# Performance work log

Hardware: AMD Instinct MI355X
Metric: run time of the kernel (lower is better)

## Reference

```python
import jax, jax.numpy as jnp
import numpy as np

N_NODES = 100000


def gcn_layer(x, ei, W, b):
    # PyG GCNConv with add_self_loops=True, edge_weight=None (all ones)
    N = x.shape[0]
    loops = jnp.arange(N, dtype=ei.dtype)
    src = jnp.concatenate([ei[0], loops])
    dst = jnp.concatenate([ei[1], loops])
    h = x @ W  # [N, out_dim]
    ones = jnp.ones(src.shape[0], dtype=x.dtype)
    deg = jax.ops.segment_sum(ones, dst, num_segments=N)
    dinv = jnp.where(deg > 0, jax.lax.rsqrt(deg), 0.0)
    norm = dinv[src] * dinv[dst]  # [E+N]
    msgs = norm[:, None] * h[src]
    out = jax.ops.segment_sum(msgs, dst, num_segments=N)
    return out + b


def forward_once(x, ei, W1, b1, W2, b2):
    h = jax.nn.relu(gcn_layer(x, ei, W1, b1))
    # Dropout(0.25) is identity in eval mode
    z = gcn_layer(h, ei, W2, b2)
    return z  # [N, embed_dim]


def setup_inputs() -> dict:
    key = jax.random.key(0)
    k = jax.random.split(key, 6)
    feat_dim, hidden_dim, embed_dim = 128, 32, 16
    R, E = 4, 1600000
    x = jax.random.normal(k[0], (N_NODES, feat_dim), dtype=jnp.float32)
    eis = jax.random.randint(k[1], (R, 2, E), 0, N_NODES, dtype=jnp.int32)
    s1 = 1.0 / np.sqrt(feat_dim)
    s2 = 1.0 / np.sqrt(hidden_dim)
    W1 = jax.random.uniform(k[2], (feat_dim, hidden_dim), jnp.float32, -s1, s1)
    b1 = jax.random.uniform(k[3], (hidden_dim,), jnp.float32, -s1, s1)
    W2 = jax.random.uniform(k[4], (hidden_dim, embed_dim), jnp.float32, -s2, s2)
    b2 = jax.random.uniform(k[5], (embed_dim,), jnp.float32, -s2, s2)
    return {"x": x, "eis": eis, "W1": W1, "b1": b1, "W2": W2, "b2": b2}


def reference(x, eis, W1, b1, W2, b2):
    # vectorize the per-relation loop over the leading R axis of eis
    embeds = jax.vmap(lambda ei: forward_once(x, ei, W1, b1, W2, b2))(eis)
    # default reduce: embeds.sum(dim=2) on [R, N, embed_dim] -> [R, N]
    return embeds.sum(axis=2)
```

## Files before the change

kernel.cpp:

```cpp
#include <hip/hip_runtime.h>


constexpr int N    = 100000;
constexpr int E    = 1600000;
constexpr int R    = 4;
constexpr int FEAT = 128;
constexpr int HID  = 32;
constexpr int EMB  = 16;
constexpr int M    = R * N;
constexpr int BS   = 256;
constexpr int SH    = 9;
constexpr int BSPAN = 1 << SH;
constexpr int NBUCK = (N + BSPAN - 1) / BSPAN;
constexpr int CH    = 4096;
constexpr int EPT   = CH / BS;
constexpr int NBKr  = (E + CH - 1) / CH;
constexpr int RB    = R * NBUCK;
constexpr int CAP   = 8960;
constexpr int SPT   = (CAP + BSPAN - 1) / BSPAN;
constexpr int OCAP  = 1536;
constexpr int FIX   = 16;
constexpr int GNB   = 64;
constexpr int XPITCH = 132;

typedef _Float16 half8 __attribute__((ext_vector_type(8)));
typedef _Float16 half2v __attribute__((ext_vector_type(2)));

__global__ __launch_bounds__(BS)
void k_gemm_h0(const float* __restrict__ x, const float* __restrict__ W1,
               _Float16* __restrict__ H0h) {
    __shared__ float xs[GNB * XPITCH];
    int base = blockIdx.x * GNB;
    int tid  = threadIdx.x;
#pragma unroll
    for (int u = 0; u < 8; ++u) {
        int f = tid + u * BS;
        int n = f >> 5;
        int c = f & 31;
        if (base + n < N) {
            float4 v = ((const float4*)(x + (size_t)(base + n) * FEAT))[c];
            int p = c ^ ((n & 7) << 2);
            *(float4*)&xs[n * XPITCH + p * 4] = v;
        }
    }
    __syncthreads();
    int oct = __builtin_amdgcn_readfirstlane(tid >> 6);
    int l   = tid & 63;
    int i   = base + l;
    const float* wp = W1 + oct * 8;
    float acc[8];
#pragma unroll
    for (int kk = 0; kk < 8; ++kk) acc[kk] = 0.f;
#pragma unroll 4
    for (int c = 0; c < 32; ++c) {
        int p = c ^ ((l & 7) << 2);
        float4 xv = *(const float4*)&xs[l * XPITCH + p * 4];
        float xk[4] = {xv.x, xv.y, xv.z, xv.w};
#pragma unroll
        for (int dk = 0; dk < 4; ++dk) {
            const float* wr = wp + (c * 4 + dk) * HID;
#pragma unroll
            for (int j = 0; j < 8; ++j)
                acc[j] = fmaf(xk[dk], wr[j], acc[j]);
        }
    }
    half8 hv;
#pragma unroll
    for (int kk = 0; kk < 8; ++kk) hv[kk] = (_Float16)acc[kk];
    if (i < N) ((half8*)H0h)[i * 4 + oct] = hv;
}

__global__ void k_wrow(const float* __restrict__ W2, const float* __restrict__ b2,
                       float* __restrict__ wrowbuf, _Float16* __restrict__ Hsc) {
    int j = threadIdx.x;
    if (j < HID) {
        float s = 0.f;
#pragma unroll
        for (int k = 0; k < EMB; ++k) s += W2[j * EMB + k];
        wrowbuf[j] = s;
    } else if (j == HID) {
        float s = 0.f;
#pragma unroll
        for (int k = 0; k < EMB; ++k) s += b2[k];
        wrowbuf[HID] = s;
    } else if (j >= 34 && j < 50) {
        ((unsigned*)(Hsc + (size_t)M * HID))[j - 34] = 0u;
    }
}

__global__ void k_scat2(const int* __restrict__ eis, int* __restrict__ gcur,
                        int* __restrict__ binned) {
    __shared__ int hist[NBUCK], lstart[NBUCK], cursor[NBUCK], gbase[NBUCK];
    __shared__ int wpart[BS / 64];
    __shared__ int shuf[CH];
    __shared__ unsigned char bkt[CH];
    int r = blockIdx.x / NBKr, k = blockIdx.x - r * NBKr;
    const int* srcp = eis + (size_t)r * 2 * E;
    const int* dstp = srcp + E;
    int e0 = k * CH, n = min(CH, E - e0);
    int tid = threadIdx.x;

    int dreg[EPT], sreg[EPT];
    if (n == CH) {
#pragma unroll
        for (int u = 0; u < EPT; ++u) {
            dreg[u] = dstp[e0 + tid + u * BS];
            sreg[u] = srcp[e0 + tid + u * BS];
        }
    } else {
#pragma unroll
        for (int u = 0; u < EPT; ++u) {
            int i = tid + u * BS;
            dreg[u] = (i < n) ? dstp[e0 + i] : -1;
            sreg[u] = (i < n) ? srcp[e0 + i] : 0;
        }
    }
    for (int b = tid; b < NBUCK; b += BS) hist[b] = 0;
    __syncthreads();
#pragma unroll
    for (int u = 0; u < EPT; ++u)
        if (dreg[u] >= 0) atomicAdd(&hist[dreg[u] >> SH], 1);
    __syncthreads();
    int v = (tid < NBUCK) ? hist[tid] : 0;
    int lanei = tid & 63;
    int s = v;
#pragma unroll
    for (int d = 1; d < 64; d <<= 1) {
        int xup = __shfl_up(s, d, 64);
        s += (lanei >= d) ? xup : 0;
    }
    if (lanei == 63) wpart[tid >> 6] = s;
    __syncthreads();
    int offw = 0;
#pragma unroll
    for (int ww = 0; ww < BS / 64; ++ww)
        offw += (ww < (tid >> 6)) ? wpart[ww] : 0;
    int ex = offw + s - v;
    if (tid < NBUCK) {
        lstart[tid] = ex;
        cursor[tid] = ex;
        gbase[tid] = atomicAdd(&gcur[r * NBUCK + tid], v);
    }
    __syncthreads();
#pragma unroll
    for (int u = 0; u < EPT; ++u) {
        int d = dreg[u];
        if (d >= 0) {
            int b = d >> SH;
            int pos = atomicAdd(&cursor[b], 1);
            shuf[pos] = ((d & (BSPAN - 1)) << 17) | sreg[u];
            bkt[pos]  = (unsigned char)b;
        }
    }
    __syncthreads();
    for (int i = tid; i < n; i += BS) {
        int b = bkt[i];
        int pos = gbase[b] + (i - lstart[b]);
        if (pos < CAP)
            binned[(size_t)(r * NBUCK + b) * CAP + pos] = shuf[i];
    }
}

__global__ __launch_bounds__(BSPAN)
void k_sort3(const int* __restrict__ gcur, int* __restrict__ binned,
             int* __restrict__ cnt, int* __restrict__ ovoff,
             float* __restrict__ dinv, const half8* __restrict__ H0h,
             half8* __restrict__ Hsc, int* __restrict__ fixedsrc) {
    __shared__ int fix_lds[FIX * BSPAN];
    __shared__ int hist[BSPAN], cur[BSPAN], oexs[BSPAN];
    __shared__ int wpart[BSPAN / 64];
    int gb = blockIdx.x;
    int r = gb / NBUCK, b = gb - r * NBUCK;
    int n = min(gcur[gb], CAP);
    int base = gb * CAP;
    int ovb  = base + (CAP - OCAP);
    int tid = threadIdx.x;
    int rg[SPT];
#pragma unroll
    for (int u = 0; u < SPT; ++u) {
        int i = tid + u * BSPAN;
        rg[u] = (i < n) ? binned[base + i] : -1;
    }
    hist[tid] = 0;
    cur[tid] = 0;
    __syncthreads();
#pragma unroll
    for (int u = 0; u < SPT; ++u)
        if (rg[u] >= 0) atomicAdd(&hist[((unsigned)rg[u]) >> 17], 1);
    __syncthreads();
    int v = hist[tid];
    int ov = max(v - FIX, 0);
    int lanei = tid & 63;
    int s = ov;
#pragma unroll
    for (int d = 1; d < 64; d <<= 1) {
        int xup = __shfl_up(s, d, 64);
        s += (lanei >= d) ? xup : 0;
    }
    if (lanei == 63) wpart[tid >> 6] = s;
    __syncthreads();
    int offw = 0;
#pragma unroll
    for (int ww = 0; ww < BSPAN / 64; ++ww)
        offw += (ww < (tid >> 6)) ? wpart[ww] : 0;
    int oex = offw + s - ov;
    oexs[tid] = oex;
    int node = (b << SH) + tid;
    int ri = r * N + node;
    if (node < N) {
        ovoff[ri] = ovb + oex;
        cnt[ri] = min(v, FIX + max(OCAP - oex, 0));
        dinv[ri] = rsqrtf((float)v + 1.0f);
    }
    __syncthreads();
#pragma unroll
    for (int u = 0; u < SPT; ++u) {
        int rc = rg[u];
        if (rc >= 0) {
            int nd = ((unsigned)rc) >> 17;
            int k = atomicAdd(&cur[nd], 1);
            int val = rc & 0x1FFFF;
            if (k < FIX) {
                fix_lds[k * BSPAN + nd] = val;
            } else {
                int p = oexs[nd] + k - FIX;
                if (p < OCAP) binned[ovb + p] = val;
            }
        }
    }
    __syncthreads();
    if (node < N) {
        int nn = min(v, FIX);
#pragma unroll
        for (int cc = 0; cc < 4; ++cc) {
            int4 w;
            w.x = (cc * 4 + 0 < nn) ? fix_lds[(cc * 4 + 0) * BSPAN + tid] : 0;
            w.y = (cc * 4 + 1 < nn) ? fix_lds[(cc * 4 + 1) * BSPAN + tid] : 0;
            w.z = (cc * 4 + 2 < nn) ? fix_lds[(cc * 4 + 2) * BSPAN + tid] : 0;
            w.w = (cc * 4 + 3 < nn) ? fix_lds[(cc * 4 + 3) * BSPAN + tid] : 0;
            ((int4*)(fixedsrc + (size_t)ri * FIX))[cc] = w;
        }
        float di = rsqrtf((float)v + 1.0f);
#pragma unroll
        for (int cc = 0; cc < 4; ++cc) {
            half8 h = H0h[(size_t)node * 4 + cc];
            half8 o;
#pragma unroll
            for (int kk = 0; kk < 8; ++kk) o[kk] = (_Float16)(di * (float)h[kk]);
            Hsc[(size_t)ri * 4 + cc] = o;
        }
    }
}

__global__ void k_l1(const int* __restrict__ cnt, const int* __restrict__ ssrc,
                     const int* __restrict__ fixedsrc, const int* __restrict__ ovoff,
                     const float* __restrict__ dinv, const half8* __restrict__ Hsc,
                     const float* __restrict__ b1, const float* __restrict__ wrowbuf,
                     float* __restrict__ q) {
    int t = blockIdx.x * blockDim.x + threadIdx.x;
    int ri = t >> 4;
    if (ri >= M) return;
    int lane = t & 15;
    int c   = lane & 3;
    int sub = lane >> 2;
    int i = ri % N;
    int rbase = ri - i;
    float di = dinv[ri];
    int n = cnt[ri];
    int fs = fixedsrc[(size_t)ri * FIX + lane];
    int base = ovoff[ri] - FIX;
    half2v acc[4];
    half2v zz = {(_Float16)0.f, (_Float16)0.f};
#pragma unroll
    for (int kk = 0; kk < 4; ++kk) acc[kk] = zz;

    auto procwin = [&](int sbv, int m) {
        for (int bq = 0; bq < 4 && bq * 4 < m; ++bq) {
            int slot = bq * 4 + sub;
            int sj = __shfl(sbv, slot, 16);
            int idx = (slot < m) ? (rbase + sj) : M;
            half8 h = Hsc[(size_t)idx * 4 + c];
#pragma unroll
            for (int kk = 0; kk < 4; ++kk) {
                half2v hp = {h[2 * kk], h[2 * kk + 1]};
                acc[kk] = acc[kk] + hp;
            }
        }
    };

    int sb = (16 + lane < n) ? ssrc[base + 16 + lane] : 0;
    procwin(fs, n);
    for (int k0 = 16; k0 < n; k0 += 16) {
        int sbn = (k0 + 16 + lane < n) ? ssrc[base + k0 + 16 + lane] : 0;
        procwin(sb, n - k0);
        sb = sbn;
    }
#pragma unroll
    for (int o = 4; o <= 8; o <<= 1) {
#pragma unroll
        for (int kk = 0; kk < 4; ++kk) {
            int av = __builtin_bit_cast(int, acc[kk]);
            av = __shfl_xor(av, o, 16);
            acc[kk] = acc[kk] + __builtin_bit_cast(half2v, av);
        }
    }
    half8 hs = Hsc[(size_t)ri * 4 + c];
#pragma unroll
    for (int kk = 0; kk < 4; ++kk) {
        half2v hp = {hs[2 * kk], hs[2 * kk + 1]};
        acc[kk] = acc[kk] + hp;
    }
    float p = 0.f;
#pragma unroll
    for (int kk = 0; kk < 8; ++kk) {
        float av = (float)acc[kk >> 1][kk & 1];
        int j = c * 8 + kk;
        float h1 = fmaf(di, av, b1[j]);
        h1 = fmaxf(h1, 0.f);
        p = fmaf(h1, wrowbuf[j], p);
    }
    p += __shfl_xor(p, 1, 16);
    p += __shfl_xor(p, 2, 16);
    if (lane == 0) q[ri] = di * p;
}

__global__ void k_l2(const int* __restrict__ cnt, const int* __restrict__ ssrc,
                     const int* __restrict__ fixedsrc, const int* __restrict__ ovoff,
                     const float* __restrict__ dinv, const float* __restrict__ q,
                     const float* __restrict__ wrowbuf, float* __restrict__ out) {
    int t = blockIdx.x * blockDim.x + threadIdx.x;
    int ri = t >> 3;
    if (ri >= M) return;
    int lane = t & 7;
    int i = ri % N;
    int rbase = ri - i;
    int n = cnt[ri];
    int f0 = fixedsrc[(size_t)ri * FIX + lane];
    int f1 = fixedsrc[(size_t)ri * FIX + 8 + lane];
    int base = ovoff[ri] - FIX;
    float val = 0.f;
    if (lane < n)     val += q[rbase + f0];
    if (8 + lane < n) val += q[rbase + f1];
    for (int idx = 16 + lane; idx < n; idx += 8) {
        int s = ssrc[base + idx];
        val += q[rbase + s];
    }
#pragma unroll
    for (int o = 4; o > 0; o >>= 1) val += __shfl_xor(val, o, 8);
    if (lane == 0)
        out[ri] = dinv[ri] * (val + q[ri]) + wrowbuf[HID];
}

extern "C" void kernel_launch(void* const* d_in, const int* in_sizes, int n_in,
                              void* d_out, int out_size, void* d_ws, size_t ws_size,
                              hipStream_t stream) {
    const float* x  = (const float*)d_in[0];
    const int*  eis = (const int*)d_in[1];
    const float* W1 = (const float*)d_in[2];
    const float* b1 = (const float*)d_in[3];
    const float* W2 = (const float*)d_in[4];
    const float* b2 = (const float*)d_in[5];
    float* out = (float*)d_out;

    _Float16* H0h = (_Float16*)d_ws;
    float* dinv   = (float*)d_ws + (size_t)N * HID / 2;
    float* q      = dinv + M;
    int*   cnt    = (int*)(q + M);
    int*   ovoff  = cnt + M;
    float* wrowbuf = (float*)(ovoff + M);
    int*   gcur   = (int*)(wrowbuf + 64);
    int*   binned = gcur + RB;
    _Float16* Hsc = (_Float16*)(binned + (size_t)RB * CAP);
    int* fixedsrc = (int*)(Hsc + (size_t)(M + 1) * HID);

    k_gemm_h0<<<(N + GNB - 1) / GNB, BS, 0, stream>>>(x, W1, H0h);
    k_wrow  <<<1, 64, 0, stream>>>(W2, b2, wrowbuf, Hsc);
    hipMemsetAsync(gcur, 0, (size_t)RB * sizeof(int), stream);
    k_scat2 <<<R * NBKr, BS, 0, stream>>>(eis, gcur, binned);
    k_sort3 <<<RB, BSPAN, 0, stream>>>(gcur, binned, cnt, ovoff, dinv,
                                       (const half8*)H0h, (half8*)Hsc, fixedsrc);
    k_l1    <<<(M * 16 + BS - 1) / BS, BS, 0, stream>>>(cnt, binned, fixedsrc,
                                                        ovoff, dinv,
                                                        (const half8*)Hsc, b1,
                                                        wrowbuf, q);
    k_l2    <<<(M * 8 + BS - 1) / BS, BS, 0, stream>>>(cnt, binned, fixedsrc,
                                                       ovoff, dinv, q, wrowbuf, out);
}
```

Baseline: 306.7 us.

## Pack per-node count, offset and dinv into one int4 metadata record

Replaces the three separate per-node arrays (cnt, ovoff, dinv) with a single int4 record, so consumers fetch one 16-byte load instead of three scattered 4-byte loads. The H0 row loads in the sort kernel and the self-feature load in layer 1 are moved earlier to overlap with other work. The scatter write-out loop gets a fully unrolled fast path for full chunks. The padded record adds some extra bytes of traffic per node, and the early loads hold more registers.

```diff
diff --git a/kernel.cpp b/kernel.cpp
--- a/kernel.cpp
+++ b/kernel.cpp
@@ -153,18 +153,28 @@
         }
     }
     __syncthreads();
-    for (int i = tid; i < n; i += BS) {
-        int b = bkt[i];
-        int pos = gbase[b] + (i - lstart[b]);
-        if (pos < CAP)
-            binned[(size_t)(r * NBUCK + b) * CAP + pos] = shuf[i];
+    if (n == CH) {
+#pragma unroll
+        for (int u = 0; u < EPT; ++u) {
+            int i = tid + u * BS;
+            int b = bkt[i];
+            int pos = gbase[b] + (i - lstart[b]);
+            if (pos < CAP)
+                binned[(size_t)(r * NBUCK + b) * CAP + pos] = shuf[i];
+        }
+    } else {
+        for (int i = tid; i < n; i += BS) {
+            int b = bkt[i];
+            int pos = gbase[b] + (i - lstart[b]);
+            if (pos < CAP)
+                binned[(size_t)(r * NBUCK + b) * CAP + pos] = shuf[i];
+        }
     }
 }
 
 __global__ __launch_bounds__(BSPAN)
 void k_sort3(const int* __restrict__ gcur, int* __restrict__ binned,
-             int* __restrict__ cnt, int* __restrict__ ovoff,
-             float* __restrict__ dinv, const half8* __restrict__ H0h,
+             int4* __restrict__ meta, const half8* __restrict__ H0h,
              half8* __restrict__ Hsc, int* __restrict__ fixedsrc) {
     __shared__ int fix_lds[FIX * BSPAN];
     __shared__ int hist[BSPAN], cur[BSPAN], oexs[BSPAN];
@@ -175,6 +185,12 @@
     int base = gb * CAP;
     int ovb  = base + (CAP - OCAP);
     int tid = threadIdx.x;
+    int node = (b << SH) + tid;
+    int ri = r * N + node;
+    int nodec = min(node, N - 1);
+    half8 h0r[4];
+#pragma unroll
+    for (int cc = 0; cc < 4; ++cc) h0r[cc] = H0h[(size_t)nodec * 4 + cc];
     int rg[SPT];
 #pragma unroll
     for (int u = 0; u < SPT; ++u) {
@@ -205,12 +221,14 @@
         offw += (ww < (tid >> 6)) ? wpart[ww] : 0;
     int oex = offw + s - ov;
     oexs[tid] = oex;
-    int node = (b << SH) + tid;
-    int ri = r * N + node;
+    float di = rsqrtf((float)v + 1.0f);
     if (node < N) {
-        ovoff[ri] = ovb + oex;
-        cnt[ri] = min(v, FIX + max(OCAP - oex, 0));
-        dinv[ri] = rsqrtf((float)v + 1.0f);
+        int4 mw;
+        mw.x = min(v, FIX + max(OCAP - oex, 0));
+        mw.y = ovb + oex;
+        mw.z = __float_as_int(di);
+        mw.w = 0;
+        meta[ri] = mw;
     }
     __syncthreads();
 #pragma unroll
@@ -240,10 +258,9 @@
             w.w = (cc * 4 + 3 < nn) ? fix_lds[(cc * 4 + 3) * BSPAN + tid] : 0;
             ((int4*)(fixedsrc + (size_t)ri * FIX))[cc] = w;
         }
-        float di = rsqrtf((float)v + 1.0f);
 #pragma unroll
         for (int cc = 0; cc < 4; ++cc) {
-            half8 h = H0h[(size_t)node * 4 + cc];
+            half8 h = h0r[cc];
             half8 o;
 #pragma unroll
             for (int kk = 0; kk < 8; ++kk) o[kk] = (_Float16)(di * (float)h[kk]);
@@ -252,9 +269,8 @@
     }
 }
 
-__global__ void k_l1(const int* __restrict__ cnt, const int* __restrict__ ssrc,
-                     const int* __restrict__ fixedsrc, const int* __restrict__ ovoff,
-                     const float* __restrict__ dinv, const half8* __restrict__ Hsc,
+__global__ void k_l1(const int4* __restrict__ meta, const int* __restrict__ ssrc,
+                     const int* __restrict__ fixedsrc, const half8* __restrict__ Hsc,
                      const float* __restrict__ b1, const float* __restrict__ wrowbuf,
                      float* __restrict__ q) {
     int t = blockIdx.x * blockDim.x + threadIdx.x;
@@ -265,10 +281,12 @@
     int sub = lane >> 2;
     int i = ri % N;
     int rbase = ri - i;
-    float di = dinv[ri];
-    int n = cnt[ri];
     int fs = fixedsrc[(size_t)ri * FIX + lane];
-    int base = ovoff[ri] - FIX;
+    half8 hs = Hsc[(size_t)ri * 4 + c];
+    int4 mo = meta[ri];
+    int n = mo.x;
+    int base = mo.y - FIX;
+    float di = __int_as_float(mo.z);
     half2v acc[4];
     half2v zz = {(_Float16)0.f, (_Float16)0.f};
 #pragma unroll
@@ -304,7 +322,6 @@
             acc[kk] = acc[kk] + __builtin_bit_cast(half2v, av);
         }
     }
-    half8 hs = Hsc[(size_t)ri * 4 + c];
 #pragma unroll
     for (int kk = 0; kk < 4; ++kk) {
         half2v hp = {hs[2 * kk], hs[2 * kk + 1]};
@@ -324,9 +341,8 @@
     if (lane == 0) q[ri] = di * p;
 }
 
-__global__ void k_l2(const int* __restrict__ cnt, const int* __restrict__ ssrc,
-                     const int* __restrict__ fixedsrc, const int* __restrict__ ovoff,
-                     const float* __restrict__ dinv, const float* __restrict__ q,
+__global__ void k_l2(const int4* __restrict__ meta, const int* __restrict__ ssrc,
+                     const int* __restrict__ fixedsrc, const float* __restrict__ q,
                      const float* __restrict__ wrowbuf, float* __restrict__ out) {
     int t = blockIdx.x * blockDim.x + threadIdx.x;
     int ri = t >> 3;
@@ -334,10 +350,11 @@
     int lane = t & 7;
     int i = ri % N;
     int rbase = ri - i;
-    int n = cnt[ri];
     int f0 = fixedsrc[(size_t)ri * FIX + lane];
     int f1 = fixedsrc[(size_t)ri * FIX + 8 + lane];
-    int base = ovoff[ri] - FIX;
+    int4 mo = meta[ri];
+    int n = mo.x;
+    int base = mo.y - FIX;
     float val = 0.f;
     if (lane < n)     val += q[rbase + f0];
     if (8 + lane < n) val += q[rbase + f1];
@@ -348,7 +365,7 @@
 #pragma unroll
     for (int o = 4; o > 0; o >>= 1) val += __shfl_xor(val, o, 8);
     if (lane == 0)
-        out[ri] = dinv[ri] * (val + q[ri]) + wrowbuf[HID];
+        out[ri] = __int_as_float(mo.z) * (val + q[ri]) + wrowbuf[HID];
 }
 
 extern "C" void kernel_launch(void* const* d_in, const int* in_sizes, int n_in,
@@ -363,11 +380,9 @@
     float* out = (float*)d_out;
 
     _Float16* H0h = (_Float16*)d_ws;
-    float* dinv   = (float*)d_ws + (size_t)N * HID / 2;
-    float* q      = dinv + M;
-    int*   cnt    = (int*)(q + M);
-    int*   ovoff  = cnt + M;
-    float* wrowbuf = (float*)(ovoff + M);
+    float* q      = (float*)d_ws + (size_t)N * HID / 2;
+    int4*  meta   = (int4*)(q + M);
+    float* wrowbuf = (float*)(meta + M);
     int*   gcur   = (int*)(wrowbuf + 64);
     int*   binned = gcur + RB;
     _Float16* Hsc = (_Float16*)(binned + (size_t)RB * CAP);
@@ -377,12 +392,11 @@
     k_wrow  <<<1, 64, 0, stream>>>(W2, b2, wrowbuf, Hsc);
     hipMemsetAsync(gcur, 0, (size_t)RB * sizeof(int), stream);
     k_scat2 <<<R * NBKr, BS, 0, stream>>>(eis, gcur, binned);
-    k_sort3 <<<RB, BSPAN, 0, stream>>>(gcur, binned, cnt, ovoff, dinv,
+    k_sort3 <<<RB, BSPAN, 0, stream>>>(gcur, binned, meta,
                                        (const half8*)H0h, (half8*)Hsc, fixedsrc);
-    k_l1    <<<(M * 16 + BS - 1) / BS, BS, 0, stream>>>(cnt, binned, fixedsrc,
-                                                        ovoff, dinv,
+    k_l1    <<<(M * 16 + BS - 1) / BS, BS, 0, stream>>>(meta, binned, fixedsrc,
                                                         (const half8*)Hsc, b1,
                                                         wrowbuf, q);
-    k_l2    <<<(M * 8 + BS - 1) / BS, BS, 0, stream>>>(cnt, binned, fixedsrc,
-                                                       ovoff, dinv, q, wrowbuf, out);
-}
+    k_l2    <<<(M * 8 + BS - 1) / BS, BS, 0, stream>>>(meta, binned, fixedsrc,
+                                                       q, wrowbuf, out);
+}
```

Measured after the change: 306.5 us (median of 2 runs). About the same (-0.1%).
